# Performance work log

Hardware: AMD Instinct MI355X
Metric: run time of the kernel (lower is better)

## Reference

```python
import jax, jax.numpy as jnp
import numpy as np

SLOTS = 64
TOPK = 1
GATE_MAX = 0.2
MEM_SCALE = 0.5
DELTA_CLIP = 2.0
LN_EPS = 1e-5


def setup_inputs() -> dict:
    key = jax.random.key(0)
    ks = jax.random.split(key, 6)
    B, T, D = 8, 4096, 896
    h = jax.random.normal(ks[0], (B, T, D), dtype=jnp.float32)
    attention_mask = jnp.ones((B, T), dtype=jnp.int32)
    ln_g = jnp.ones((D,), dtype=jnp.float32)
    ln_b = jnp.zeros((D,), dtype=jnp.float32)
    W_out = (jax.random.normal(ks[1], (D, D), dtype=jnp.float32) * 0.02)      # mem_out: Linear(D,D,bias=False)
    W_nm = (jax.random.normal(ks[2], (1, 2 * D), dtype=jnp.float32) * 0.02)   # neuromod: Linear(2D,1)
    b_nm = jnp.zeros((1,), dtype=jnp.float32)
    W_wg = (jax.random.normal(ks[3], (1, D + 1), dtype=jnp.float32) * 0.02)   # write_gate: Linear(D+1,1)
    b_wg = jnp.zeros((1,), dtype=jnp.float32)
    return dict(h=h, attention_mask=attention_mask, ln_g=ln_g, ln_b=ln_b,
                W_out=W_out, W_nm=W_nm, b_nm=b_nm, W_wg=W_wg, b_wg=b_wg)


def reference(h, attention_mask, ln_g, ln_b, W_out, W_nm, b_nm, W_wg, b_wg):
    B, T, D = h.shape
    scale = 1.0 / jnp.sqrt(jnp.float32(D))
    mem_k0 = jnp.zeros((B, SLOTS, D), dtype=jnp.float32)
    mem_v0 = jnp.zeros((B, SLOTS, D), dtype=jnp.float32)
    keep = attention_mask.astype(jnp.float32)
    batch_idx = jnp.arange(B)[:, None]

    def step(carry, xs):
        mem_k, mem_v = carry
        h_t, keep_t = xs                                   # [B,D], [B]
        # content-based read: attention over slots
        scores = jnp.einsum('bd,bsd->bs', h_t, mem_k) * scale
        attn = jax.nn.softmax(scores, axis=-1)
        m = jnp.einsum('bs,bsd->bd', attn, mem_v)          # [B,D]
        # neuromodulator gate
        g = jax.nn.sigmoid(jnp.concatenate([h_t, m], axis=-1) @ W_nm.T + b_nm)   # [B,1]
        # write gate, clamped and masked by attention mask
        wg = jax.nn.sigmoid(jnp.concatenate([h_t, g], axis=-1) @ W_wg.T + b_wg)  # [B,1]
        wg = jnp.clip(wg, 0.0, GATE_MAX) * keep_t[:, None]
        # top-k gated write with straight-through selection
        soft = jax.nn.softmax(scores, axis=-1)             # address by content similarity
        _, idx = jax.lax.top_k(soft, TOPK)                 # [B,TOPK]
        hard = jnp.zeros_like(soft).at[batch_idx, idx].set(1.0 / TOPK)
        w = hard + soft - jax.lax.stop_gradient(soft)      # straight-through weights [B,S]
        gw = (wg * w)[..., None]                           # [B,S,1]
        mem_k = mem_k * (1.0 - gw) + gw * h_t[:, None, :]
        mem_v = mem_v * (1.0 - gw) + gw * h_t[:, None, :]
        # memory residual: LN -> Linear -> scale -> clip
        mu = jnp.mean(m, axis=-1, keepdims=True)
        var = jnp.var(m, axis=-1, keepdims=True)
        mn = (m - mu) / jnp.sqrt(var + LN_EPS) * ln_g + ln_b
        delta = jnp.clip((mn @ W_out.T) * MEM_SCALE, -DELTA_CLIP, DELTA_CLIP)
        return (mem_k, mem_v), h_t + delta

    xs = (jnp.swapaxes(h, 0, 1), jnp.swapaxes(keep, 0, 1))  # time-major for scan
    (_, _), h2 = jax.lax.scan(step, (mem_k0, mem_v0), xs)
    return jnp.swapaxes(h2, 0, 1)                          # [B,T,D]
```

## Files before the change

### kernel.cpp

```cpp
#include <hip/hip_runtime.h>
#include <hip/hip_bf16.h>

#define DIM 896
#define TT 4096
#define BB 8
#define NS 64
#define CC 128
#define NC 32
#define RCH 256
#define NRC 16
#define NSLICE 14

typedef float floatx4 __attribute__((ext_vector_type(4)));
typedef short short8 __attribute__((ext_vector_type(8)));

#define DPP_F(x_, ctrl_, rmask_, old_) \
  __int_as_float(__builtin_amdgcn_update_dpp(__float_as_int(old_), __float_as_int(x_), (ctrl_), (rmask_), 0xf, false))

__device__ __forceinline__ float wave_sum64(float x) {
    x += DPP_F(x, 0x111, 0xf, 0.0f);
    x += DPP_F(x, 0x112, 0xf, 0.0f);
    x += DPP_F(x, 0x114, 0xf, 0.0f);
    x += DPP_F(x, 0x118, 0xf, 0.0f);
    x += DPP_F(x, 0x142, 0xa, 0.0f);
    x += DPP_F(x, 0x143, 0xc, 0.0f);
    return __int_as_float(__builtin_amdgcn_readlane(__float_as_int(x), 63));
}
__device__ __forceinline__ float wave_max64(float x) {
    x = fmaxf(x, DPP_F(x, 0x111, 0xf, -INFINITY));
    x = fmaxf(x, DPP_F(x, 0x112, 0xf, -INFINITY));
    x = fmaxf(x, DPP_F(x, 0x114, 0xf, -INFINITY));
    x = fmaxf(x, DPP_F(x, 0x118, 0xf, -INFINITY));
    x = fmaxf(x, DPP_F(x, 0x142, 0xa, -INFINITY));
    x = fmaxf(x, DPP_F(x, 0x143, 0xc, -INFINITY));
    return __int_as_float(__builtin_amdgcn_readlane(__float_as_int(x), 63));
}

__device__ __forceinline__ float rfl_f(float x) {
    return __int_as_float(__builtin_amdgcn_readfirstlane(__float_as_int(x)));
}
__device__ __forceinline__ float rl_f(float x, int l) {
    return __int_as_float(__builtin_amdgcn_readlane(__float_as_int(x), l));
}

__global__ __launch_bounds__(64) void k0_dots(const float* __restrict__ h,
                                              const float* __restrict__ W_nm,
                                              const float* __restrict__ W_wg,
                                              float* __restrict__ R, float* __restrict__ Q,
                                              float* __restrict__ P2) {
    const int r = blockIdx.x;
    const int lane = threadIdx.x;
    const float2* hr = (const float2*)(h + (size_t)r * DIM);
    const float2* w0 = (const float2*)W_nm;
    const float2* w1 = (const float2*)(W_nm + DIM);
    const float2* w2 = (const float2*)W_wg;
    float a = 0.f, bsum = 0.f, c = 0.f;
    #pragma unroll
    for (int i = 0; i < 7; ++i) {
        int idx = lane + 64 * i;
        float2 hv = hr[idx];
        float2 a0 = w0[idx], a1 = w1[idx], a2 = w2[idx];
        a = fmaf(hv.x, a0.x, fmaf(hv.y, a0.y, a));
        bsum = fmaf(hv.x, a1.x, fmaf(hv.y, a1.y, bsum));
        c = fmaf(hv.x, a2.x, fmaf(hv.y, a2.y, c));
    }
    #pragma unroll
    for (int off = 32; off; off >>= 1) {
        a += __shfl_xor(a, off);
        bsum += __shfl_xor(bsum, off);
        c += __shfl_xor(c, off);
    }
    if (lane == 0) { R[r] = a; P2[r] = bsum; Q[r] = c; }
}

__global__ __launch_bounds__(256) void kG_gram(const float* __restrict__ h,
                                               float* __restrict__ Gd, int part) {
    const int blk = blockIdx.x + part * 128;
    const int bc = blk >> 1, half = blk & 1;
    const int b = bc / NC, c = bc % NC;
    const int tid = threadIdx.x;
    const int ti = tid >> 4, tj = tid & 15;
    __shared__ float Hs[32][132];
    float acc[8][4];
    #pragma unroll
    for (int u = 0; u < 8; u++)
        #pragma unroll
        for (int v = 0; v < 4; v++) acc[u][v] = 0.f;
    const size_t hb = (size_t)b * TT * DIM + (size_t)c * CC * DIM;
    for (int kb = 0; kb < 28; ++kb) {
        __syncthreads();
        #pragma unroll
        for (int l = 0; l < 4; ++l) {
            int idx = tid + l * 256;
            int r = idx >> 3, kq = idx & 7;
            float4 f = *(const float4*)&h[hb + (size_t)r * DIM + kb * 32 + kq * 4];
            Hs[kq * 4 + 0][r] = f.x; Hs[kq * 4 + 1][r] = f.y;
            Hs[kq * 4 + 2][r] = f.z; Hs[kq * 4 + 3][r] = f.w;
        }
        __syncthreads();
        #pragma unroll 4
        for (int k = 0; k < 32; ++k) {
            float4 a0 = *(const float4*)&Hs[k][ti * 8];
            float4 a1 = *(const float4*)&Hs[k][ti * 8 + 4];
            float4 bv = *(const float4*)&Hs[k][half * 64 + tj * 4];
            float av[8] = {a0.x, a0.y, a0.z, a0.w, a1.x, a1.y, a1.z, a1.w};
            float bb[4] = {bv.x, bv.y, bv.z, bv.w};
            #pragma unroll
            for (int u = 0; u < 8; u++)
                #pragma unroll
                for (int v = 0; v < 4; v++)
                    acc[u][v] = fmaf(av[u], bb[v], acc[u][v]);
        }
    }
    float* gp = Gd + (size_t)bc * CC * CC;
    #pragma unroll
    for (int u = 0; u < 8; u++) {
        float4 o = {acc[u][0], acc[u][1], acc[u][2], acc[u][3]};
        *(float4*)&gp[(size_t)(ti * 8 + u) * CC + half * 64 + tj * 4] = o;
    }
}

#define MC_(i) case i: mc[i] = fmaf(mc[i], om, wh); break;
__global__ __launch_bounds__(256) void kB_base(const float* __restrict__ h,
                                               const float* __restrict__ wgbuf,
                                               const int* __restrict__ ssbuf,
                                               float* __restrict__ memS,
                                               float* __restrict__ snap,
                                               float* __restrict__ Bpart,
                                               int c) {
    const int slice = blockIdx.x;
    const int b = blockIdx.y;
    const int tid = threadIdx.x;
    __shared__ float wsh[CC];
    __shared__ int   ssh[CC];
    __shared__ float Asb[64][65];
    __shared__ float Bsb[CC][65];

    if (tid < CC) {
        wsh[tid] = wgbuf[b * TT + (c - 1) * CC + tid];
        ssh[tid] = ssbuf[b * TT + (c - 1) * CC + tid];
    }
    const int q = tid >> 6, d = tid & 63;
    const int dg = slice * 64 + d;
    float mc[16];
    #pragma unroll
    for (int j = 0; j < 16; j++) mc[j] = memS[((size_t)b * NS + q * 16 + j) * DIM + dg];
    __syncthreads();

    const size_t hb = (size_t)b * TT * DIM + (size_t)((c - 1) * CC) * DIM + dg;
    float hv[16];
    #pragma unroll
    for (int j = 0; j < 16; ++j) hv[j] = h[hb + (size_t)j * DIM];
    for (int i0 = 0; i0 < CC; i0 += 16) {
        float hvn[16];
        if (i0 + 16 < CC) {
            #pragma unroll
            for (int j = 0; j < 16; ++j) hvn[j] = h[hb + (size_t)(i0 + 16 + j) * DIM];
        }
        #pragma unroll
        for (int j = 0; j < 16; ++j) {
            const int i = i0 + j;
            float hvv = hv[j];
            int ss = __builtin_amdgcn_readfirstlane(ssh[i]);
            float w = rfl_f(wsh[i]);
            if ((ss >> 4) == q) {
                float om = 1.f - w, wh = w * hvv;
                switch (ss & 15) {
                    MC_(0) MC_(1) MC_(2) MC_(3) MC_(4) MC_(5) MC_(6) MC_(7)
                    MC_(8) MC_(9) MC_(10) MC_(11) MC_(12) MC_(13) MC_(14) MC_(15)
                }
            }
        }
        #pragma unroll
        for (int j = 0; j < 16; ++j) hv[j] = hvn[j];
    }
    #pragma unroll
    for (int j = 0; j < 16; j++) {
        memS[((size_t)b * NS + q * 16 + j) * DIM + dg] = mc[j];
        Asb[d][q * 16 + j] = mc[j];
    }
    if ((c & 1) == 0) {
        const int r = c >> 1;
        #pragma unroll
        for (int j = 0; j < 16; j++)
            snap[(((size_t)b * NRC + r) * NS + q * 16 + j) * DIM + dg] = mc[j];
    }
    const size_t hb2 = (size_t)b * TT * DIM + (size_t)(c * CC) * DIM + slice * 64;
    for (int idx = tid; idx < CC * 64; idx += 256) {
        int tp = idx >> 6, k = idx & 63;
        Bsb[tp][k] = h[hb2 + (size_t)tp * DIM + k];
    }
    __syncthreads();

    const int tg = tid >> 3, sg = tid & 7;
    float acc[4][8];
    #pragma unroll
    for (int v = 0; v < 4; v++)
        #pragma unroll
        for (int u = 0; u < 8; u++) acc[v][u] = 0.f;
    #pragma unroll 4
    for (int k = 0; k < 64; ++k) {
        float bv[4], av[8];
        #pragma unroll
        for (int v = 0; v < 4; v++) bv[v] = Bsb[tg * 4 + v][k];
        #pragma unroll
        for (int u = 0; u < 8; u++) av[u] = Asb[k][sg * 8 + u];
        #pragma unroll
        for (int v = 0; v < 4; v++)
            #pragma unroll
            for (int u = 0; u < 8; u++)
                acc[v][u] = fmaf(bv[v], av[u], acc[v][u]);
    }
    float* bp = Bpart + ((size_t)(slice * BB + b)) * CC * NS;
    #pragma unroll
    for (int v = 0; v < 4; v++) {
        float4 o0 = {acc[v][0], acc[v][1], acc[v][2], acc[v][3]};
        float4 o1 = {acc[v][4], acc[v][5], acc[v][6], acc[v][7]};
        *(float4*)&bp[(size_t)(tg * 4 + v) * NS + sg * 8] = o0;
        *(float4*)&bp[(size_t)(tg * 4 + v) * NS + sg * 8 + 4] = o1;
    }
}

#define SIDX(r, c_) (((r) << 6) + (((c_) ^ ((r) & 63))))
__global__ __launch_bounds__(256) void kS_seq(const float* __restrict__ Bpart,
                                              const float* __restrict__ Gd,
                                              const float* __restrict__ Rv,
                                              const float* __restrict__ Qv,
                                              const float* __restrict__ P2v,
                                              const int* __restrict__ mask,
                                              const float* __restrict__ b_nm,
                                              const float* __restrict__ b_wg,
                                              const float* __restrict__ W_wg,
                                              float* __restrict__ Kvec,
                                              float* __restrict__ fbuf,
                                              float* __restrict__ wgbuf,
                                              int* __restrict__ ssbuf,
                                              int c) {
    const int b = blockIdx.x;
    const int tid = threadIdx.x;
    const int lane = tid & 63;
    const int wv = tid >> 6;
    __shared__ float S[129 * 64];
    __shared__ float Gb[2][17 * 128];
    const int tb = b * TT + c * CC;
    const float* gdc = Gd + (size_t)(b * NC + c) * CC * CC;

    if (c == 0) {
        for (int t = wv * 32; t < wv * 32 + 32; ++t) S[SIDX(t, lane)] = 0.f;
    } else {
        const float* bp0 = Bpart + (size_t)b * CC * NS;
        for (int t = wv * 32; t < wv * 32 + 32; ++t) {
            float s = 0.f;
            #pragma unroll
            for (int sl = 0; sl < NSLICE; ++sl)
                s += bp0[(size_t)sl * (BB * CC * NS) + (size_t)t * NS + lane];
            S[SIDX(t, lane)] = s;
        }
    }
    for (int idx = tid; idx < 512; idx += 256) {
        int r = idx >> 5, cq = idx & 31;
        *(float4*)&Gb[0][r * 128 + cq * 4] = *(const float4*)&gdc[(size_t)r * CC + cq * 4];
    }

    float cur = 0.f, p1 = 0.f, p2 = 0.f, p3 = 0.f, K = 0.f;
    float Rl0 = 0.f, Rl1 = 0.f, Ql0 = 0.f, Ql1 = 0.f;
    float Pl0 = 0.f, Pl1 = 0.f, Ml0 = 0.f, Ml1 = 0.f;
    float bnm = 0.f, bwg = 0.f, wD = 0.f;
    const float scale = 1.0f / sqrtf((float)DIM);
    if (wv == 0) {
        cur = S[SIDX(0, lane)];
        p1  = S[SIDX(1, lane)];
        p2  = S[SIDX(2, lane)];
        p3  = S[SIDX(3, lane)];
        K = Kvec[b * NS + lane];
        Rl0 = Rv[tb + lane];  Rl1 = Rv[tb + 64 + lane];
        Ql0 = Qv[tb + lane];  Ql1 = Qv[tb + 64 + lane];
        Pl0 = P2v[tb + lane]; Pl1 = P2v[tb + 64 + lane];
        Ml0 = (float)mask[tb + lane]; Ml1 = (float)mask[tb + 64 + lane];
        bnm = b_nm[0]; bwg = b_wg[0]; wD = W_wg[DIM];
    }
    __syncthreads();

    for (int bb = 0; bb < 8; ++bb) {
        if (wv == 0) {
            const int base = bb * 16;
            const float* gcur = Gb[bb & 1];
            const float Rb = (base & 64) ? Rl1 : Rl0;
            const float Qb = (base & 64) ? Ql1 : Ql0;
            const float Pb = (base & 64) ? Pl1 : Pl0;
            const float Mb = (base & 64) ? Ml1 : Ml0;
            float g0 = gcur[(base + 1 + lane) & 127];
            float g1 = gcur[(base + 65 + lane) & 127];
            #pragma unroll 4
            for (int s = 0; s < 16; ++s) {
                const int tau = base + s;
                float g0n = gcur[(s + 1) * 128 + ((tau + 2 + lane) & 127)];
                float g1n = gcur[(s + 1) * 128 + ((tau + 66 + lane) & 127)];
                int rp4 = tau + 4; rp4 = (rp4 > 128) ? 128 : rp4;
                float p4 = S[SIDX(rp4, lane)];
                const float Rt = rl_f(Rb, tau & 63);
                const float Qt = rl_f(Qb, tau & 63);
                const float Pt = rl_f(Pb, tau & 63);
                const float Mk = rl_f(Mb, tau & 63);

                float sco = cur * scale;
                float mv = wave_max64(sco);
                float e = __expf(sco);
                float se = wave_sum64(e);
                float sk = wave_sum64(e * K);
                unsigned long long bal = __ballot(sco == mv);
                int mi = (int)__ffsll(bal) - 1;

                float inv = 1.f / se;
                fbuf[((size_t)tb + tau) * NS + lane] = e * inv;
                float gdot = sk * inv;
                float g = 1.f / (1.f + __expf(-(Rt + gdot + bnm)));
                float w = 1.f / (1.f + __expf(-(Qt + g * wD + bwg)));
                w = fminf(w, 0.2f) * Mk;
                if (lane == 0) {
                    wgbuf[tb + tau] = w;
                    ssbuf[tb + tau] = mi;
                }
                float om = 1.f - w;
                K = (lane == mi) ? fmaf(K, om, w * Pt) : K;

                int r1 = tau + 1 + lane;
                int ix1 = (lane >= 4 && r1 < 128) ? SIDX(r1, mi) : (128 * 64 + lane);
                int r2 = tau + 65 + lane;
                int ix2 = (r2 < 128) ? SIDX(r2, mi) : (128 * 64 + lane);
                S[ix1] = fmaf(S[ix1], om, w * g0);
                S[ix2] = fmaf(S[ix2], om, w * g1);

                const float q1 = rl_f(g0, 0), q2 = rl_f(g0, 1);
                const float q3 = rl_f(g0, 2), q4 = rl_f(g0, 3);
                const bool m_ = (lane == mi);
                p1 = m_ ? fmaf(p1, om, w * q1) : p1;
                p2 = m_ ? fmaf(p2, om, w * q2) : p2;
                p3 = m_ ? fmaf(p3, om, w * q3) : p3;
                p4 = m_ ? fmaf(p4, om, w * q4) : p4;
                cur = p1; p1 = p2; p2 = p3; p3 = p4;
                g0 = g0n; g1 = g1n;
            }
        } else if (bb < 7) {
            const int bs = (bb + 1) * 16;
            float* dst = Gb[(bb + 1) & 1];
            for (int idx = tid - 64; idx < 512; idx += 192) {
                int r = idx >> 5, cq = idx & 31;
                *(float4*)&dst[r * 128 + cq * 4] =
                    *(const float4*)&gdc[(size_t)(bs + r) * CC + cq * 4];
            }
        }
        __syncthreads();
    }
    if (wv == 0) Kvec[b * NS + lane] = K;
}

__global__ __launch_bounds__(256) void k1_wcvt(const float* __restrict__ W,
                                               __hip_bfloat16* __restrict__ Wb) {
    const int idx = blockIdx.x * 256 + threadIdx.x;
    const float4 f = ((const float4*)W)[idx];
    alignas(8) __hip_bfloat16 t[4];
    t[0] = __float2bfloat16(f.x); t[1] = __float2bfloat16(f.y);
    t[2] = __float2bfloat16(f.z); t[3] = __float2bfloat16(f.w);
    *(uint2*)&Wb[(size_t)idx * 4] = *(const uint2*)t;
}

#define CS_(i) case i: mem[i] = fmaf(mem[i], sA, aB); break;
__global__ __launch_bounds__(448) void k2_replay(const float* __restrict__ h,
                                                 const float* __restrict__ fbuf,
                                                 const float* __restrict__ wgbuf,
                                                 const int* __restrict__ ssbuf,
                                                 const float* __restrict__ snap,
                                                 __hip_bfloat16* __restrict__ Mbuf,
                                                 int part) {
    const int blk = blockIdx.x + part * 64;
    const int b = blk >> 5;
    const int c = (blk >> 1) & 15;
    const int halfD = blk & 1;
    const int tid = threadIdx.x;
    const int dg = halfD * 448 + tid;

    __shared__ float lf[128 * NS];
    __shared__ float lwg[RCH];
    __shared__ int   lss[RCH];

    float mem[64];
    const float* sp = snap + (((size_t)b * NRC + c) * NS) * DIM + dg;
    #pragma unroll
    for (int s2 = 0; s2 < 64; s2++) mem[s2] = sp[(size_t)s2 * DIM];

    const int t0 = c * RCH;
    if (tid < RCH) {
        lwg[tid] = wgbuf[b * TT + t0 + tid];
        lss[tid] = ssbuf[b * TT + t0 + tid];
    }
    const size_t hbase = (size_t)b * TT * DIM + (size_t)t0 * DIM + dg;
    const size_t fbase = ((size_t)b * TT + t0) * NS;
    const size_t mrow = ((size_t)b * TT + t0) * DIM + dg;

    for (int half = 0; half < 2; ++half) {
        __syncthreads();
        const float4* src = (const float4*)(fbuf + fbase + (size_t)half * 128 * NS);
        for (int idx = tid; idx < 128 * NS / 4; idx += 448)
            ((float4*)lf)[idx] = src[idx];
        __syncthreads();

        float hv[8];
        #pragma unroll
        for (int j = 0; j < 8; ++j)
            hv[j] = h[hbase + (size_t)(half * 128 + j) * DIM];

        for (int tg = 0; tg < 128; tg += 8) {
            float hvn[8];
            if (tg + 8 < 128) {
                #pragma unroll
                for (int j = 0; j < 8; ++j)
                    hvn[j] = h[hbase + (size_t)(half * 128 + tg + 8 + j) * DIM];
            }
            #pragma unroll
            for (int j = 0; j < 8; ++j) {
                const int tl = tg + j;
                const int tt = half * 128 + tl;
                const float4* f4p = (const float4*)&lf[tl * NS];
                float m0 = 0.f, m1 = 0.f, m2 = 0.f, m3 = 0.f;
                #pragma unroll
                for (int qq = 0; qq < 16; qq++) {
                    float4 f4 = f4p[qq];
                    m0 = fmaf(f4.x, mem[4 * qq], m0);
                    m1 = fmaf(f4.y, mem[4 * qq + 1], m1);
                    m2 = fmaf(f4.z, mem[4 * qq + 2], m2);
                    m3 = fmaf(f4.w, mem[4 * qq + 3], m3);
                }
                Mbuf[mrow + (size_t)tt * DIM] = __float2bfloat16((m0 + m1) + (m2 + m3));
                int ss = __builtin_amdgcn_readfirstlane(lss[tt]);
                float w = rfl_f(lwg[tt]);
                float sA = 1.0f - w, aB = w * hv[j];
                switch (ss) {
                    CS_(0) CS_(1) CS_(2) CS_(3) CS_(4) CS_(5) CS_(6) CS_(7)
                    CS_(8) CS_(9) CS_(10) CS_(11) CS_(12) CS_(13) CS_(14) CS_(15)
                    CS_(16) CS_(17) CS_(18) CS_(19) CS_(20) CS_(21) CS_(22) CS_(23)
                    CS_(24) CS_(25) CS_(26) CS_(27) CS_(28) CS_(29) CS_(30) CS_(31)
                    CS_(32) CS_(33) CS_(34) CS_(35) CS_(36) CS_(37) CS_(38) CS_(39)
                    CS_(40) CS_(41) CS_(42) CS_(43) CS_(44) CS_(45) CS_(46) CS_(47)
                    CS_(48) CS_(49) CS_(50) CS_(51) CS_(52) CS_(53) CS_(54) CS_(55)
                    CS_(56) CS_(57) CS_(58) CS_(59) CS_(60) CS_(61) CS_(62) CS_(63)
                }
            }
            #pragma unroll
            for (int j = 0; j < 8; ++j) hv[j] = hvn[j];
        }
    }
}

__global__ __launch_bounds__(64) void k3_ln(__hip_bfloat16* __restrict__ Mbuf,
                                            const float* __restrict__ ln_g,
                                            const float* __restrict__ ln_b) {
    const size_t r = blockIdx.x;
    const int lane = threadIdx.x;
    __hip_bfloat162* row2 = (__hip_bfloat162*)(Mbuf + r * DIM);
    float vx[7], vy[7];
    float s1 = 0.f, s2 = 0.f;
    #pragma unroll
    for (int i = 0; i < 7; i++) {
        __hip_bfloat162 x2 = row2[lane + 64 * i];
        float x = __bfloat162float(x2.x), y = __bfloat162float(x2.y);
        vx[i] = x; vy[i] = y;
        s1 += x + y;
        s2 = fmaf(x, x, fmaf(y, y, s2));
    }
    #pragma unroll
    for (int off = 32; off; off >>= 1) {
        s1 += __shfl_xor(s1, off);
        s2 += __shfl_xor(s2, off);
    }
    float mu = s1 * (1.0f / DIM);
    float var = fmaxf(s2 * (1.0f / DIM) - mu * mu, 0.0f);
    float rs = 1.0f / sqrtf(var + 1e-5f);
    #pragma unroll
    for (int i = 0; i < 7; i++) {
        int d = 2 * (lane + 64 * i);
        float2 lg = *(const float2*)&ln_g[d];
        float2 lb = *(const float2*)&ln_b[d];
        __hip_bfloat162 o;
        o.x = __float2bfloat16((vx[i] - mu) * rs * lg.x + lb.x);
        o.y = __float2bfloat16((vy[i] - mu) * rs * lg.y + lb.y);
        row2[lane + 64 * i] = o;
    }
}

__global__ __launch_bounds__(256) void k4_gemm(const __hip_bfloat16* __restrict__ Mn,
                                               const __hip_bfloat16* __restrict__ Wb,
                                               const float* __restrict__ h,
                                               float* __restrict__ out) {
    const int nt = blockIdx.x;
    const int mt = blockIdx.y;
    const int tid = threadIdx.x;
    const int wave = tid >> 6, lane = tid & 63;
    const int wr = wave >> 1, wc = wave & 1;

    __shared__ __hip_bfloat16 Asb[128 * 72];
    __shared__ __hip_bfloat16 Bsb[128 * 72];

    floatx4 acc[4][4];
    #pragma unroll
    for (int i = 0; i < 4; i++)
        #pragma unroll
        for (int jn = 0; jn < 4; jn++)
            acc[i][jn] = (floatx4){0.f, 0.f, 0.f, 0.f};

    const int lrow = lane & 15;
    const int lk = (lane >> 4) * 8;
    const int rr = tid >> 3, ch = tid & 7;

    for (int kt = 0; kt < 14; ++kt) {
        #pragma unroll
        for (int it = 0; it < 4; ++it) {
            int row = rr + 32 * it;
            const uint4* srcA = (const uint4*)(Mn + ((size_t)(mt * 128 + row)) * DIM + kt * 64 + ch * 8);
            *(uint4*)&Asb[row * 72 + ch * 8] = *srcA;
            const uint4* srcB = (const uint4*)(Wb + ((size_t)(nt * 128 + row)) * DIM + kt * 64 + ch * 8);
            *(uint4*)&Bsb[row * 72 + ch * 8] = *srcB;
        }
        __syncthreads();
        #pragma unroll
        for (int kk = 0; kk < 2; ++kk) {
            short8 af[4], bfr[4];
            #pragma unroll
            for (int i = 0; i < 4; i++)
                af[i] = *(const short8*)&Asb[(wr * 64 + i * 16 + lrow) * 72 + kk * 32 + lk];
            #pragma unroll
            for (int i2 = 0; i2 < 4; i2++)
                bfr[i2] = *(const short8*)&Bsb[(wc * 64 + i2 * 16 + lrow) * 72 + kk * 32 + lk];
            #pragma unroll
            for (int i = 0; i < 4; i++)
                #pragma unroll
                for (int jn = 0; jn < 4; jn++)
                    acc[i][jn] = __builtin_amdgcn_mfma_f32_16x16x32_bf16(af[i], bfr[jn], acc[i][jn], 0, 0, 0);
        }
        __syncthreads();
    }
    const int crow = (lane >> 4) * 4, ccol = lane & 15;
    #pragma unroll
    for (int i = 0; i < 4; i++)
        #pragma unroll
        for (int jn = 0; jn < 4; jn++)
            #pragma unroll
            for (int rg = 0; rg < 4; rg++) {
                int rG = mt * 128 + wr * 64 + i * 16 + crow + rg;
                int nG = nt * 128 + wc * 64 + jn * 16 + ccol;
                size_t idx = (size_t)rG * DIM + nG;
                float d = acc[i][jn][rg] * 0.5f;
                d = fminf(fmaxf(d, -2.0f), 2.0f);
                out[idx] = h[idx] + d;
            }
}

extern "C" void kernel_launch(void* const* d_in, const int* in_sizes, int n_in,
                              void* d_out, int out_size, void* d_ws, size_t ws_size,
                              hipStream_t stream) {
    const float* h      = (const float*)d_in[0];
    const int* mask     = (const int*)d_in[1];
    const float* ln_g   = (const float*)d_in[2];
    const float* ln_b   = (const float*)d_in[3];
    const float* W_out  = (const float*)d_in[4];
    const float* W_nm   = (const float*)d_in[5];
    const float* b_nm   = (const float*)d_in[6];
    const float* W_wg   = (const float*)d_in[7];
    const float* b_wg   = (const float*)d_in[8];
    float* out = (float*)d_out;

    char* ws = (char*)d_ws;
    float* Bpart = (float*)(ws);
    float* memS  = (float*)(ws + 8388608);
    float* Kvec  = (float*)(ws + 8388608 + 1835008);
    float* snap  = (float*)(ws + 8388608 + 1835008 + 2048);
    const size_t Z0 = 8388608;
    const size_t ZBYTES = 1835008 + 2048 + 29360128;
    float* fbuf  = (float*)(ws + 8388608 + ZBYTES);
    float* wgbuf = (float*)(ws + 8388608 + ZBYTES + 8388608);
    int*   ssbuf = (int*)  (ws + 8388608 + ZBYTES + 8388608 + 131072);
    char*  Mreg  = ws + 8388608 + ZBYTES + 8388608 + 262144;
    float* Gd = (float*)(Mreg);
    float* R  = (float*)(Mreg + 16777216);
    float* Q  = (float*)(Mreg + 16777216 + 131072);
    float* P2 = (float*)(Mreg + 16777216 + 262144);
    __hip_bfloat16* Mbuf = (__hip_bfloat16*)Mreg;
    __hip_bfloat16* Wb = (__hip_bfloat16*)(ws);

    hipMemsetAsync(ws + Z0, 0, ZBYTES, stream);
    hipLaunchKernelGGL(k0_dots, dim3(BB * TT), dim3(64), 0, stream,
                       h, W_nm, W_wg, R, Q, P2);
    for (int p = 0; p < 4; ++p)
        hipLaunchKernelGGL(kG_gram, dim3(128), dim3(256), 0, stream, h, Gd, p);

    hipLaunchKernelGGL(kS_seq, dim3(BB), dim3(256), 0, stream,
                       Bpart, Gd, R, Q, P2, mask, b_nm, b_wg, W_wg,
                       Kvec, fbuf, wgbuf, ssbuf, 0);
    for (int c = 1; c < NC; ++c) {
        hipLaunchKernelGGL(kB_base, dim3(NSLICE, BB), dim3(256), 0, stream,
                           h, wgbuf, ssbuf, memS, snap, Bpart, c);
        hipLaunchKernelGGL(kS_seq, dim3(BB), dim3(256), 0, stream,
                           Bpart, Gd, R, Q, P2, mask, b_nm, b_wg, W_wg,
                           Kvec, fbuf, wgbuf, ssbuf, c);
    }

    hipLaunchKernelGGL(k1_wcvt, dim3(784), dim3(256), 0, stream, W_out, Wb);
    for (int p = 0; p < 4; ++p)
        hipLaunchKernelGGL(k2_replay, dim3(64), dim3(448), 0, stream,
                           h, fbuf, wgbuf, ssbuf, snap, Mbuf, p);
    hipLaunchKernelGGL(k3_ln, dim3(BB * TT), dim3(64), 0, stream,
                       Mbuf, ln_g, ln_b);
    hipLaunchKernelGGL(k4_gemm, dim3(7, 256), dim3(256), 0, stream,
                       Mbuf, Wb, h, out);
}
```

Baseline: 4.605 ms.

## Batch replay reads over eight steps with delta corrections and merge partitioned launches

The replay kernel now computes the memory read dot products for eight timesteps from the memory state at the start of each group. It then applies small rank-one corrections for the slot writes made earlier in the group before each read is emitted. This breaks the serial dependence between each read and the previous write, which should expose more instruction-level parallelism. The gram and replay kernels also move from four partitioned launches each to one full-grid launch, cutting launch overhead and letting blocks run concurrently. The cost is extra LDS reads and FMAs for the corrections, plus a slightly different floating-point summation order.

```diff
diff --git a/kernel.cpp b/kernel.cpp
--- a/kernel.cpp
+++ b/kernel.cpp
@@ -74,8 +74,8 @@
 }
 
 __global__ __launch_bounds__(256) void kG_gram(const float* __restrict__ h,
-                                               float* __restrict__ Gd, int part) {
-    const int blk = blockIdx.x + part * 128;
+                                               float* __restrict__ Gd) {
+    const int blk = blockIdx.x;
     const int bc = blk >> 1, half = blk & 1;
     const int b = bc / NC, c = bc % NC;
     const int tid = threadIdx.x;
@@ -365,15 +365,14 @@
     *(uint2*)&Wb[(size_t)idx * 4] = *(const uint2*)t;
 }
 
-#define CS_(i) case i: mem[i] = fmaf(mem[i], sA, aB); break;
+#define CS_(i) case i: { float ov = mem[i]; float nv = fmaf(ov, sA, aB); mem[i] = nv; dj = nv - ov; } break;
 __global__ __launch_bounds__(448) void k2_replay(const float* __restrict__ h,
                                                  const float* __restrict__ fbuf,
                                                  const float* __restrict__ wgbuf,
                                                  const int* __restrict__ ssbuf,
                                                  const float* __restrict__ snap,
-                                                 __hip_bfloat16* __restrict__ Mbuf,
-                                                 int part) {
-    const int blk = blockIdx.x + part * 64;
+                                                 __hip_bfloat16* __restrict__ Mbuf) {
+    const int blk = blockIdx.x;
     const int b = blk >> 5;
     const int c = (blk >> 1) & 15;
     const int halfD = blk & 1;
@@ -417,11 +416,10 @@
                 for (int j = 0; j < 8; ++j)
                     hvn[j] = h[hbase + (size_t)(half * 128 + tg + 8 + j) * DIM];
             }
+            float bm[8];
             #pragma unroll
             for (int j = 0; j < 8; ++j) {
-                const int tl = tg + j;
-                const int tt = half * 128 + tl;
-                const float4* f4p = (const float4*)&lf[tl * NS];
+                const float4* f4p = (const float4*)&lf[(tg + j) * NS];
                 float m0 = 0.f, m1 = 0.f, m2 = 0.f, m3 = 0.f;
                 #pragma unroll
                 for (int qq = 0; qq < 16; qq++) {
@@ -431,10 +429,24 @@
                     m2 = fmaf(f4.z, mem[4 * qq + 2], m2);
                     m3 = fmaf(f4.w, mem[4 * qq + 3], m3);
                 }
-                Mbuf[mrow + (size_t)tt * DIM] = __float2bfloat16((m0 + m1) + (m2 + m3));
+                bm[j] = (m0 + m1) + (m2 + m3);
+            }
+            int   ssg[8];
+            float dlt[8];
+            #pragma unroll
+            for (int j = 0; j < 8; ++j) {
+                const int tt = half * 128 + tg + j;
+                float m = bm[j];
+                #pragma unroll
+                for (int j2 = 0; j2 < 8; ++j2) {
+                    if (j2 < j)
+                        m = fmaf(lf[(tg + j) * NS + ssg[j2]], dlt[j2], m);
+                }
+                Mbuf[mrow + (size_t)tt * DIM] = __float2bfloat16(m);
                 int ss = __builtin_amdgcn_readfirstlane(lss[tt]);
                 float w = rfl_f(lwg[tt]);
                 float sA = 1.0f - w, aB = w * hv[j];
+                float dj = 0.f;
                 switch (ss) {
                     CS_(0) CS_(1) CS_(2) CS_(3) CS_(4) CS_(5) CS_(6) CS_(7)
                     CS_(8) CS_(9) CS_(10) CS_(11) CS_(12) CS_(13) CS_(14) CS_(15)
@@ -445,6 +457,8 @@
                     CS_(48) CS_(49) CS_(50) CS_(51) CS_(52) CS_(53) CS_(54) CS_(55)
                     CS_(56) CS_(57) CS_(58) CS_(59) CS_(60) CS_(61) CS_(62) CS_(63)
                 }
+                ssg[j] = ss;
+                dlt[j] = dj;
             }
             #pragma unroll
             for (int j = 0; j < 8; ++j) hv[j] = hvn[j];
@@ -590,8 +604,7 @@
     hipMemsetAsync(ws + Z0, 0, ZBYTES, stream);
     hipLaunchKernelGGL(k0_dots, dim3(BB * TT), dim3(64), 0, stream,
                        h, W_nm, W_wg, R, Q, P2);
-    for (int p = 0; p < 4; ++p)
-        hipLaunchKernelGGL(kG_gram, dim3(128), dim3(256), 0, stream, h, Gd, p);
+    hipLaunchKernelGGL(kG_gram, dim3(BB * NC * 2), dim3(256), 0, stream, h, Gd);
 
     hipLaunchKernelGGL(kS_seq, dim3(BB), dim3(256), 0, stream,
                        Bpart, Gd, R, Q, P2, mask, b_nm, b_wg, W_wg,
@@ -605,9 +618,8 @@
     }
 
     hipLaunchKernelGGL(k1_wcvt, dim3(784), dim3(256), 0, stream, W_out, Wb);
-    for (int p = 0; p < 4; ++p)
-        hipLaunchKernelGGL(k2_replay, dim3(64), dim3(448), 0, stream,
-                           h, fbuf, wgbuf, ssbuf, snap, Mbuf, p);
+    hipLaunchKernelGGL(k2_replay, dim3(BB * NRC * 2), dim3(448), 0, stream,
+                       h, fbuf, wgbuf, ssbuf, snap, Mbuf);
     hipLaunchKernelGGL(k3_ln, dim3(BB * TT), dim3(64), 0, stream,
                        Mbuf, ln_g, ln_b);
     hipLaunchKernelGGL(k4_gemm, dim3(7, 256), dim3(256), 0, stream,
```

Result: slower. 6.683 ms (+45.1%).
